# Optimization experiments

Hardware: AMD Instinct MI355X
Metric: run time of the kernel (lower is better)

The kernel has to match this reference:

```python
import jax, jax.numpy as jnp
import numpy as np

EMBED_DIM = 1024
HEAD_NUM = 16
NEG = 100000.0


def setup_inputs() -> dict:
    key = jax.random.key(0)
    k1, k2, k3, k4, k5 = jax.random.split(key, 5)
    B, S, E = 2, 2048, EMBED_DIM
    return {
        "x": jax.random.normal(k1, (B, S, E), dtype=jnp.float32),
        "w_attn": jax.random.normal(k2, (E, 3 * E), dtype=jnp.float32) * 0.02,
        "b_attn": jax.random.normal(k3, (3 * E,), dtype=jnp.float32) * 0.02,
        "w_proj": jax.random.normal(k4, (E, E), dtype=jnp.float32) * 0.02,
        "b_proj": jax.random.normal(k5, (E,), dtype=jnp.float32) * 0.02,
    }


def reference(x, w_attn, b_attn, w_proj, b_proj):
    B, S, E = x.shape
    H = HEAD_NUM
    d = E // H
    dk = jnp.asarray(d, x.dtype) ** 0.5  # (embed_dim // head_num) ** 0.5

    qkv = x @ w_attn + b_attn                      # [B, S, 3E]
    qkv = qkv.reshape(B, S, H, 3 * d)              # split heads BEFORE chunk (as in source)
    qkv = jnp.swapaxes(qkv, 1, 2)                  # [B, H, S, 3d]
    q, k, v = jnp.split(qkv, 3, axis=-1)           # each [B, H, S, d]

    w = jnp.einsum("bhqd,bhkd->bhqk", q, k) / dk   # [B, H, S, S]
    mask = jnp.tril(jnp.ones((S, S), dtype=x.dtype))
    w = w * mask - (1.0 - mask) * NEG              # exact masking math of source
    w = jax.nn.softmax(w, axis=-1)                 # dropout omitted (eval mode)

    a = jnp.einsum("bhqk,bhkd->bhqd", w, v)        # [B, H, S, d]
    a = jnp.swapaxes(a, 1, 2).reshape(B, S, E)     # [B, S, E]
    h = a @ w_proj + b_proj                        # resi dropout omitted (eval mode)
    return h
```

## Files before the change

kernel.cpp:

```cpp
#include <hip/hip_runtime.h>
#include <hip/hip_bf16.h>

#define BB 2
#define SS 2048
#define EE 1024
#define HH 16
#define DD 64
#define MM (BB*SS)
#define N1 (3*EE)

typedef __attribute__((ext_vector_type(4))) float f32x4;
typedef __attribute__((ext_vector_type(16))) float f32x16;
typedef __attribute__((ext_vector_type(8))) short bf16x8;
typedef __attribute__((ext_vector_type(4))) unsigned int u32x4;
typedef __attribute__((ext_vector_type(2))) unsigned int u32x2;

__device__ __forceinline__ ushort f2bf(float f){
  union { float f; unsigned u; } v; v.f = f;
  unsigned r = v.u + 0x7fffu + ((v.u >> 16) & 1u);
  return (ushort)(r >> 16);
}

__device__ __forceinline__ unsigned cvt_pk(float a, float b){
  unsigned r; asm("v_cvt_pk_bf16_f32 %0, %1, %2" : "=v"(r) : "v"(a), "v"(b)); return r;
}

__device__ __forceinline__ float exp2_fast(float x){
  float r; asm("v_exp_f32 %0, %1" : "=v"(r) : "v"(x)); return r;
}

__device__ __forceinline__ u32x2 pl32swap(unsigned a, unsigned b){
  return __builtin_amdgcn_permlane32_swap(a, b, false, false);
}

__device__ __forceinline__ void gload16(const void* g, void* l){
  __builtin_amdgcn_global_load_lds(
      (const __attribute__((address_space(1))) unsigned*)g,
      (__attribute__((address_space(3))) unsigned*)l, 16, 0, 0);
}

__global__ __launch_bounds__(256) void prep_kernel(const float* __restrict__ x, ushort* __restrict__ xb,
    const float* __restrict__ wa, ushort* __restrict__ waT,
    const float* __restrict__ wp, ushort* __restrict__ wpT){
  __shared__ float t[32][33];
  const int bid = blockIdx.x, tid = threadIdx.x;
  if (bid < 4096){
    int i = bid*256 + tid;
    const float4 f = reinterpret_cast<const float4*>(x)[i];
    ushort4 o; o.x=f2bf(f.x); o.y=f2bf(f.y); o.z=f2bf(f.z); o.w=f2bf(f.w);
    reinterpret_cast<ushort4*>(xb)[i] = o;
  } else {
    const float* in; ushort* out; int N, nx, b;
    if (bid < 7168){ b = bid - 4096; in = wa; out = waT; N = N1; nx = N1/32; }
    else           { b = bid - 7168; in = wp; out = wpT; N = EE; nx = EE/32; }
    const int n0 = (b % nx)*32, k0 = (b / nx)*32;
    const int tx = tid & 31, ty = tid >> 5;
    for (int r = ty; r < 32; r += 8)
      t[r][tx] = in[(size_t)(k0+r)*N + n0 + tx];
    __syncthreads();
    for (int r = ty; r < 32; r += 8)
      out[(size_t)(n0+r)*EE + k0 + tx] = f2bf(t[tx][r]);
  }
}

template<int MODE>
__global__ __launch_bounds__(256) void gemm_nt(const ushort* __restrict__ A,
    const ushort* __restrict__ Bt, const float* __restrict__ bias,
    ushort* __restrict__ q_, ushort* __restrict__ k_, ushort* __restrict__ v_,
    float* __restrict__ of, int M, int N, int K){
  __shared__ ushort As[128*32];
  __shared__ ushort Bs[128*32];
  const int tid = threadIdx.x;
  const int lane = tid & 63, w = tid >> 6;
  const int nx = gridDim.x;
  const int nwg = nx * gridDim.y;
  const int flat = blockIdx.y*nx + blockIdx.x;
  const int sw = (flat & 7)*(nwg >> 3) + (flat >> 3);
  const int m0 = (sw / nx)*128, n0 = (sw % nx)*128;
  const int wm = (w >> 1)*64, wn = (w & 1)*64;
  const int lr = lane & 15, lk = (lane >> 4)*8;
  const int c0 = w*2;
  const int srow = lane >> 2;
  const int scb  = (lane & 3)*8;
  const ushort* Ag0 = A  + (size_t)(m0 + c0*16      + srow)*K + scb;
  const ushort* Ag1 = A  + (size_t)(m0 + c0*16 + 16 + srow)*K + scb;
  const ushort* Bg0 = Bt + (size_t)(n0 + c0*16      + srow)*K + scb;
  const ushort* Bg1 = Bt + (size_t)(n0 + c0*16 + 16 + srow)*K + scb;
  ushort* Al0 = &As[(c0*16)*32];
  ushort* Al1 = &As[(c0*16 + 16)*32];
  ushort* Bl0 = &Bs[(c0*16)*32];
  ushort* Bl1 = &Bs[(c0*16 + 16)*32];

  f32x4 acc[4][4] = {};
  for (int k0 = 0; k0 < K; k0 += 32){
    gload16(Ag0 + k0, Al0);
    gload16(Ag1 + k0, Al1);
    gload16(Bg0 + k0, Bl0);
    gload16(Bg1 + k0, Bl1);
    __syncthreads();
    bf16x8 af[4], bfr[4];
    #pragma unroll
    for (int m = 0; m < 4; ++m)
      af[m] = *reinterpret_cast<bf16x8*>(&As[(wm + m*16 + lr)*32 + lk]);
    #pragma unroll
    for (int n = 0; n < 4; ++n)
      bfr[n] = *reinterpret_cast<bf16x8*>(&Bs[(wn + n*16 + lr)*32 + lk]);
    __builtin_amdgcn_s_setprio(1);
    #pragma unroll
    for (int m = 0; m < 4; ++m)
      #pragma unroll
      for (int n = 0; n < 4; ++n)
        acc[m][n] = __builtin_amdgcn_mfma_f32_16x16x32_bf16(af[m], bfr[n], acc[m][n], 0, 0, 0);
    __builtin_amdgcn_s_setprio(0);
    __syncthreads();
  }
  #pragma unroll
  for (int m = 0; m < 4; ++m){
    #pragma unroll
    for (int n = 0; n < 4; ++n){
      int col = n0 + wn + n*16 + lr;
      float bv = bias[col];
      #pragma unroll
      for (int r = 0; r < 4; ++r){
        int row = m0 + wm + m*16 + (lane >> 4)*4 + r;
        float v = acc[m][n][r] + bv;
        if (MODE == 1){
          of[(size_t)row*N + col] = v;
        } else {
          int b = row >> 11, s = row & 2047;
          int h = col / 192, t = col - h*192;
          ushort u = f2bf(v);
          size_t bh = (size_t)(b*HH + h);
          if (t < 64)       q_[(bh*SS + s)*DD + t]        = u;
          else if (t < 128) k_[(bh*SS + s)*DD + (t-64)]   = u;
          else              v_[(bh*DD + (t-128))*SS + s]  = u;
        }
      }
    }
  }
}

#define SCL 0.18033688f
#define THRRAW 44.3614f
__global__ __launch_bounds__(256,2) void attn2(const ushort* __restrict__ Qg,
    const ushort* __restrict__ Kg, const ushort* __restrict__ Vg,
    ushort* __restrict__ aout){
  __shared__ __align__(16) ushort Kl[4][64*64];
  __shared__ __align__(16) ushort Vl[4][64*64];
  const int tid = threadIdx.x, lane = tid & 63, w = tid >> 6;
  const int bh = blockIdx.x;
  const int y  = blockIdx.y;
  const int qt = (y < 8) ? 2*y : 31 - 2*y;
  const int b = bh >> 4, h = bh & 15;
  const int q0 = qt*128;
  const int ql = lane & 31, g = lane >> 5;
  const int qrow = q0 + w*32 + ql;
  const int qminw = q0 + w*32;
  const int qmaxw = qminw + 31;

  const ushort* Qp = Qg + ((size_t)bh*SS + qrow)*DD;
  bf16x8 qf[4];
  #pragma unroll
  for (int s = 0; s < 4; ++s)
    qf[s] = *(const bf16x8*)(Qp + s*16 + g*8);

  f32x16 ot[2] = {};
  float mr = -1e30f, sr = 0.f;

  const int csr = lane >> 3;
  const int gcb = ((lane & 7) ^ csr)*8;
  const ushort* Kbase = Kg + (size_t)bh*SS*DD;
  const ushort* Vbase = Vg + (size_t)bh*DD*SS;
  const int nkb = (q0 + 128) >> 6;
  const int nv  = (qmaxw >> 6) + 1;
  const int swq = (ql & 7);

  auto stage = [&](int t){
    const int k0 = t*64, bi = t & 3;
    #pragma unroll
    for (int i = 0; i < 2; ++i){
      const int c = w*2 + i;
      gload16(Kbase + (size_t)(k0 + c*8 + csr)*DD + gcb, &Kl[bi][(c*8)*64]);
      gload16(Vbase + (size_t)(c*8 + csr)*SS + k0 + gcb, &Vl[bi][(c*8)*64]);
    }
  };

  auto qk = [&](int t, f32x16& s0, f32x16& s1){
    const ushort* Kc = &Kl[t & 3][0];
    f32x16 a0 = {}, a1 = {};
    __builtin_amdgcn_s_setprio(1);
    #pragma unroll
    for (int s = 0; s < 4; ++s){
      bf16x8 kf0 = *(const bf16x8*)&Kc[ ql     *64 + (((2*s + g) ^ swq)*8)];
      bf16x8 kf1 = *(const bf16x8*)&Kc[(32+ql) *64 + (((2*s + g) ^ swq)*8)];
      a0 = __builtin_amdgcn_mfma_f32_32x32x16_bf16(kf0, qf[s], a0, 0, 0, 0);
      a1 = __builtin_amdgcn_mfma_f32_32x32x16_bf16(kf1, qf[s], a1, 0, 0, 0);
    }
    __builtin_amdgcn_s_setprio(0);
    const int k0 = t*64;
    if (k0 + 63 > qminw){
      #pragma unroll
      for (int r = 0; r < 16; ++r){
        int kg0 = k0 + (r & 3) + 8*(r >> 2) + 4*g;
        a0[r] = (kg0 > qrow) ? -1e30f : a0[r];
        a1[r] = (kg0 + 32 > qrow) ? -1e30f : a1[r];
      }
    }
    s0 = a0; s1 = a1;
  };

  auto smpv = [&](int t, f32x16& s0, f32x16& s1){
    float p[2][16];
    #pragma unroll
    for (int r = 0; r < 16; ++r){ p[0][r] = s0[r]; p[1][r] = s1[r]; }
    float m8[8];
    #pragma unroll
    for (int i = 0; i < 8; ++i)
      m8[i] = fmaxf(fmaxf(p[0][i], p[0][i+8]), fmaxf(p[1][i], p[1][i+8]));
    float tm = fmaxf(fmaxf(fmaxf(m8[0],m8[1]), fmaxf(m8[2],m8[3])),
                     fmaxf(fmaxf(m8[4],m8[5]), fmaxf(m8[6],m8[7])));
    { u32x2 rm = pl32swap(__float_as_uint(tm), __float_as_uint(tm));
      tm = fmaxf(__uint_as_float(rm[0]), __uint_as_float(rm[1])); }
    if (__any(tm > mr + THRRAW)){
      float nm = fmaxf(mr, tm);
      float fac = exp2_fast((mr - nm)*SCL);
      #pragma unroll
      for (int r = 0; r < 16; ++r){ ot[0][r] *= fac; ot[1][r] *= fac; }
      sr *= fac;
      mr = nm;
    }
    const float nms = mr * SCL;
    #pragma unroll
    for (int kf = 0; kf < 2; ++kf)
      #pragma unroll
      for (int r = 0; r < 16; ++r)
        p[kf][r] = exp2_fast(__builtin_fmaf(p[kf][r], SCL, -nms));
    float s8[8];
    #pragma unroll
    for (int i = 0; i < 8; ++i)
      s8[i] = (p[0][i] + p[0][i+8]) + (p[1][i] + p[1][i+8]);
    float ts = ((s8[0]+s8[1]) + (s8[2]+s8[3])) + ((s8[4]+s8[5]) + (s8[6]+s8[7]));
    { u32x2 rs = pl32swap(__float_as_uint(ts), __float_as_uint(ts));
      ts = __uint_as_float(rs[0]) + __uint_as_float(rs[1]); }
    sr += ts;

    const ushort* Vc = &Vl[t & 3][0];
    __builtin_amdgcn_s_setprio(1);
    #pragma unroll
    for (int kf = 0; kf < 2; ++kf){
      #pragma unroll
      for (int s2 = 0; s2 < 2; ++s2){
        const int base = s2*8;
        unsigned u0 = cvt_pk(p[kf][base+0], p[kf][base+1]);
        unsigned u1 = cvt_pk(p[kf][base+2], p[kf][base+3]);
        unsigned u2 = cvt_pk(p[kf][base+4], p[kf][base+5]);
        unsigned u3 = cvt_pk(p[kf][base+6], p[kf][base+7]);
        u32x2 r0 = pl32swap(u0, u2);
        u32x2 r1 = pl32swap(u1, u3);
        union { u32x4 u; bf16x8 hv; } pw;
        pw.u[0] = r0[0]; pw.u[1] = r1[0]; pw.u[2] = r0[1]; pw.u[3] = r1[1];
        const int cbv = 4*kf + 2*s2 + g;
        bf16x8 v0f = *(const bf16x8*)&Vc[ ql     *64 + ((cbv ^ swq)*8)];
        bf16x8 v1f = *(const bf16x8*)&Vc[(32+ql) *64 + ((cbv ^ swq)*8)];
        ot[0] = __builtin_amdgcn_mfma_f32_32x32x16_bf16(v0f, pw.hv, ot[0], 0, 0, 0);
        ot[1] = __builtin_amdgcn_mfma_f32_32x32x16_bf16(v1f, pw.hv, ot[1], 0, 0, 0);
      }
    }
    __builtin_amdgcn_s_setprio(0);
  };

  stage(0);
  stage(1);
  f32x16 pA0, pA1, pB0, pB1;
  for (int tt = 0; tt < nkb; tt += 2){
    asm volatile("s_waitcnt vmcnt(4)" ::: "memory");
    __builtin_amdgcn_s_barrier();
    __builtin_amdgcn_sched_barrier(0);
    if (tt + 2 < nkb) stage(tt + 2);
    if (tt < nv) qk(tt, pA0, pA1);
    if (tt > 0 && tt - 1 < nv) smpv(tt - 1, pB0, pB1);
    if (tt + 2 < nkb) { asm volatile("s_waitcnt vmcnt(4)" ::: "memory"); }
    else              { asm volatile("s_waitcnt vmcnt(0)" ::: "memory"); }
    __builtin_amdgcn_s_barrier();
    __builtin_amdgcn_sched_barrier(0);
    if (tt + 3 < nkb) stage(tt + 3);
    if (tt + 1 < nv) qk(tt + 1, pB0, pB1);
    if (tt < nv) smpv(tt, pA0, pA1);
  }
  if (nkb - 1 < nv) smpv(nkb - 1, pB0, pB1);

  const float inv = 1.f / sr;
  const size_t obase = ((size_t)b*SS + qrow)*EE + h*DD;
  #pragma unroll
  for (int df = 0; df < 2; ++df){
    #pragma unroll
    for (int t = 0; t < 4; ++t){
      ushort4 o4;
      o4.x = f2bf(ot[df][t*4+0]*inv);
      o4.y = f2bf(ot[df][t*4+1]*inv);
      o4.z = f2bf(ot[df][t*4+2]*inv);
      o4.w = f2bf(ot[df][t*4+3]*inv);
      int d = df*32 + 8*t + 4*g;
      *(ushort4*)&aout[obase + d] = o4;
    }
  }
}

extern "C" void kernel_launch(void* const* d_in, const int* in_sizes, int n_in,
                              void* d_out, int out_size, void* d_ws, size_t ws_size,
                              hipStream_t stream){
  const float* x      = (const float*)d_in[0];
  const float* w_attn = (const float*)d_in[1];
  const float* b_attn = (const float*)d_in[2];
  const float* w_proj = (const float*)d_in[3];
  const float* b_proj = (const float*)d_in[4];
  float* out = (float*)d_out;

  ushort* ws   = (ushort*)d_ws;
  ushort* xb   = ws;
  ushort* waT  = xb  + (size_t)MM*EE;
  ushort* wpT  = waT + (size_t)N1*EE;
  ushort* qb_  = wpT + (size_t)EE*EE;
  ushort* kb_  = qb_ + (size_t)MM*EE;
  ushort* vTb  = kb_ + (size_t)MM*EE;
  ushort* ab   = vTb + (size_t)MM*EE;

  prep_kernel<<<8192, 256, 0, stream>>>(x, xb, w_attn, waT, w_proj, wpT);
  gemm_nt<0><<<dim3(N1/128, MM/128), 256, 0, stream>>>(xb, waT, b_attn, qb_, kb_, vTb, nullptr, MM, N1, EE);
  attn2<<<dim3(BB*HH, SS/128), 256, 0, stream>>>(qb_, kb_, vTb, ab);
  gemm_nt<1><<<dim3(EE/128, MM/128), 256, 0, stream>>>(ab, wpT, b_proj, nullptr, nullptr, nullptr, out, MM, EE, EE);
}
```

Baseline: 123.4 us.

## Pair causal query tiles per attention block and deepen GEMM K-tile with swizzle

The attention kernel now launches 512-thread blocks where two 4-wave groups handle complementary causal query tiles (u and 15-u). They share one K/V staging pipeline that covers the longer tile's range, which balances work and halves K/V global loads per pair. The GEMM moves from a K-tile of 32 to 64 with XOR-swizzled LDS layout, halving barriers per K and cutting bank conflicts. Tradeoffs are doubled GEMM LDS use and lower attention occupancy (one 512-thread block per CU via launch bounds). The shorter group also sits through barriers for blocks it does not need.

```diff
diff --git a/kernel.cpp b/kernel.cpp
--- a/kernel.cpp
+++ b/kernel.cpp
@@ -68,8 +68,8 @@
     const ushort* __restrict__ Bt, const float* __restrict__ bias,
     ushort* __restrict__ q_, ushort* __restrict__ k_, ushort* __restrict__ v_,
     float* __restrict__ of, int M, int N, int K){
-  __shared__ ushort As[128*32];
-  __shared__ ushort Bs[128*32];
+  __shared__ ushort As[128*64];
+  __shared__ ushort Bs[128*64];
   const int tid = threadIdx.x;
   const int lane = tid & 63, w = tid >> 6;
   const int nx = gridDim.x;
@@ -78,40 +78,38 @@
   const int sw = (flat & 7)*(nwg >> 3) + (flat >> 3);
   const int m0 = (sw / nx)*128, n0 = (sw % nx)*128;
   const int wm = (w >> 1)*64, wn = (w & 1)*64;
-  const int lr = lane & 15, lk = (lane >> 4)*8;
-  const int c0 = w*2;
-  const int srow = lane >> 2;
-  const int scb  = (lane & 3)*8;
-  const ushort* Ag0 = A  + (size_t)(m0 + c0*16      + srow)*K + scb;
-  const ushort* Ag1 = A  + (size_t)(m0 + c0*16 + 16 + srow)*K + scb;
-  const ushort* Bg0 = Bt + (size_t)(n0 + c0*16      + srow)*K + scb;
-  const ushort* Bg1 = Bt + (size_t)(n0 + c0*16 + 16 + srow)*K + scb;
-  ushort* Al0 = &As[(c0*16)*32];
-  ushort* Al1 = &As[(c0*16 + 16)*32];
-  ushort* Bl0 = &Bs[(c0*16)*32];
-  ushort* Bl1 = &Bs[(c0*16 + 16)*32];
+  const int lr = lane & 15, g4 = lane >> 4;
+  const int c0 = w*4;
+  const int csr = lane >> 3;
+  const int gcb = ((lane & 7) ^ csr)*8;
+  const int sw7 = lr & 7;
 
   f32x4 acc[4][4] = {};
-  for (int k0 = 0; k0 < K; k0 += 32){
-    gload16(Ag0 + k0, Al0);
-    gload16(Ag1 + k0, Al1);
-    gload16(Bg0 + k0, Bl0);
-    gload16(Bg1 + k0, Bl1);
+  for (int k0 = 0; k0 < K; k0 += 64){
+    #pragma unroll
+    for (int i = 0; i < 4; ++i){
+      const int c = c0 + i;
+      gload16(A  + (size_t)(m0 + c*8 + csr)*K + k0 + gcb, &As[(c*8)*64]);
+      gload16(Bt + (size_t)(n0 + c*8 + csr)*K + k0 + gcb, &Bs[(c*8)*64]);
+    }
     __syncthreads();
-    bf16x8 af[4], bfr[4];
-    #pragma unroll
-    for (int m = 0; m < 4; ++m)
-      af[m] = *reinterpret_cast<bf16x8*>(&As[(wm + m*16 + lr)*32 + lk]);
-    #pragma unroll
-    for (int n = 0; n < 4; ++n)
-      bfr[n] = *reinterpret_cast<bf16x8*>(&Bs[(wn + n*16 + lr)*32 + lk]);
-    __builtin_amdgcn_s_setprio(1);
-    #pragma unroll
-    for (int m = 0; m < 4; ++m)
+    #pragma unroll
+    for (int kk = 0; kk < 2; ++kk){
+      bf16x8 af[4], bfr[4];
+      #pragma unroll
+      for (int m = 0; m < 4; ++m)
+        af[m] = *reinterpret_cast<bf16x8*>(&As[(wm + m*16 + lr)*64 + (((kk*4 + g4) ^ sw7)*8)]);
       #pragma unroll
       for (int n = 0; n < 4; ++n)
-        acc[m][n] = __builtin_amdgcn_mfma_f32_16x16x32_bf16(af[m], bfr[n], acc[m][n], 0, 0, 0);
-    __builtin_amdgcn_s_setprio(0);
+        bfr[n] = *reinterpret_cast<bf16x8*>(&Bs[(wn + n*16 + lr)*64 + (((kk*4 + g4) ^ sw7)*8)]);
+      __builtin_amdgcn_s_setprio(1);
+      #pragma unroll
+      for (int m = 0; m < 4; ++m)
+        #pragma unroll
+        for (int n = 0; n < 4; ++n)
+          acc[m][n] = __builtin_amdgcn_mfma_f32_16x16x32_bf16(af[m], bfr[n], acc[m][n], 0, 0, 0);
+      __builtin_amdgcn_s_setprio(0);
+    }
     __syncthreads();
   }
   #pragma unroll
@@ -142,20 +140,21 @@
 
 #define SCL 0.18033688f
 #define THRRAW 44.3614f
-__global__ __launch_bounds__(256,2) void attn2(const ushort* __restrict__ Qg,
+__global__ __launch_bounds__(512,1) void attn2(const ushort* __restrict__ Qg,
     const ushort* __restrict__ Kg, const ushort* __restrict__ Vg,
     ushort* __restrict__ aout){
   __shared__ __align__(16) ushort Kl[4][64*64];
   __shared__ __align__(16) ushort Vl[4][64*64];
   const int tid = threadIdx.x, lane = tid & 63, w = tid >> 6;
   const int bh = blockIdx.x;
-  const int y  = blockIdx.y;
-  const int qt = (y < 8) ? 2*y : 31 - 2*y;
+  const int u  = blockIdx.y;
+  const int G  = w >> 2, wv = w & 3;
+  const int qt = G ? (15 - u) : u;
   const int b = bh >> 4, h = bh & 15;
   const int q0 = qt*128;
   const int ql = lane & 31, g = lane >> 5;
-  const int qrow = q0 + w*32 + ql;
-  const int qminw = q0 + w*32;
+  const int qrow = q0 + wv*32 + ql;
+  const int qminw = q0 + wv*32;
   const int qmaxw = qminw + 31;
 
   const ushort* Qp = Qg + ((size_t)bh*SS + qrow)*DD;
@@ -171,18 +170,14 @@
   const int gcb = ((lane & 7) ^ csr)*8;
   const ushort* Kbase = Kg + (size_t)bh*SS*DD;
   const ushort* Vbase = Vg + (size_t)bh*DD*SS;
-  const int nkb = (q0 + 128) >> 6;
-  const int nv  = (qmaxw >> 6) + 1;
+  const int nkbL = 2*(16 - u);
+  const int nv   = (qmaxw >> 6) + 1;
   const int swq = (ql & 7);
 
   auto stage = [&](int t){
     const int k0 = t*64, bi = t & 3;
-    #pragma unroll
-    for (int i = 0; i < 2; ++i){
-      const int c = w*2 + i;
-      gload16(Kbase + (size_t)(k0 + c*8 + csr)*DD + gcb, &Kl[bi][(c*8)*64]);
-      gload16(Vbase + (size_t)(c*8 + csr)*SS + k0 + gcb, &Vl[bi][(c*8)*64]);
-    }
+    gload16(Kbase + (size_t)(k0 + w*8 + csr)*DD + gcb, &Kl[bi][(w*8)*64]);
+    gload16(Vbase + (size_t)(w*8 + csr)*SS + k0 + gcb, &Vl[bi][(w*8)*64]);
   };
 
   auto qk = [&](int t, f32x16& s0, f32x16& s1){
@@ -272,22 +267,22 @@
   stage(0);
   stage(1);
   f32x16 pA0, pA1, pB0, pB1;
-  for (int tt = 0; tt < nkb; tt += 2){
-    asm volatile("s_waitcnt vmcnt(4)" ::: "memory");
+  for (int tt = 0; tt < nkbL; tt += 2){
+    asm volatile("s_waitcnt vmcnt(2)" ::: "memory");
     __builtin_amdgcn_s_barrier();
     __builtin_amdgcn_sched_barrier(0);
-    if (tt + 2 < nkb) stage(tt + 2);
+    if (tt + 2 < nkbL) stage(tt + 2);
     if (tt < nv) qk(tt, pA0, pA1);
     if (tt > 0 && tt - 1 < nv) smpv(tt - 1, pB0, pB1);
-    if (tt + 2 < nkb) { asm volatile("s_waitcnt vmcnt(4)" ::: "memory"); }
-    else              { asm volatile("s_waitcnt vmcnt(0)" ::: "memory"); }
+    if (tt + 2 < nkbL) { asm volatile("s_waitcnt vmcnt(2)" ::: "memory"); }
+    else               { asm volatile("s_waitcnt vmcnt(0)" ::: "memory"); }
     __builtin_amdgcn_s_barrier();
     __builtin_amdgcn_sched_barrier(0);
-    if (tt + 3 < nkb) stage(tt + 3);
+    if (tt + 3 < nkbL) stage(tt + 3);
     if (tt + 1 < nv) qk(tt + 1, pB0, pB1);
     if (tt < nv) smpv(tt, pA0, pA1);
   }
-  if (nkb - 1 < nv) smpv(nkb - 1, pB0, pB1);
+  if (nkbL - 1 < nv) smpv(nkbL - 1, pB0, pB1);
 
   const float inv = 1.f / sr;
   const size_t obase = ((size_t)b*SS + qrow)*EE + h*DD;
@@ -327,6 +322,6 @@
 
   prep_kernel<<<8192, 256, 0, stream>>>(x, xb, w_attn, waT, w_proj, wpT);
   gemm_nt<0><<<dim3(N1/128, MM/128), 256, 0, stream>>>(xb, waT, b_attn, qb_, kb_, vTb, nullptr, MM, N1, EE);
-  attn2<<<dim3(BB*HH, SS/128), 256, 0, stream>>>(qb_, kb_, vTb, ab);
+  attn2<<<dim3(BB*HH, 8), 512, 0, stream>>>(qb_, kb_, vTb, ab);
   gemm_nt<1><<<dim3(EE/128, MM/128), 256, 0, stream>>>(ab, wpT, b_proj, nullptr, nullptr, nullptr, out, MM, EE, EE);
 }
```

Result: faster. 118.0 us (-4.4%).
